# Performance work log

Hardware: AMD Instinct MI355X
Metric: run time of the kernel (lower is better)

The kernel has to match this reference:

```python
import math
import jax, jax.numpy as jnp
import numpy as np

B, T, E, NH = 2, 4096, 768, 12
HS = E // NH

def setup_inputs() -> dict:
    key = jax.random.key(0)
    k1, k2, k3 = jax.random.split(key, 3)
    x = jax.random.normal(k1, (B, T, E), dtype=jnp.float32)
    W_attn = jax.random.normal(k2, (E, 3 * E), dtype=jnp.float32) * (1.0 / math.sqrt(E))
    b_attn = jnp.zeros((3 * E,), dtype=jnp.float32)
    W_proj = jax.random.normal(k3, (E, E), dtype=jnp.float32) * (1.0 / math.sqrt(E))
    b_proj = jnp.zeros((E,), dtype=jnp.float32)
    return {"x": x, "W_attn": W_attn, "b_attn": b_attn, "W_proj": W_proj, "b_proj": b_proj}

def reference(x, W_attn, b_attn, W_proj, b_proj):
    b, t, e = x.shape
    nh, hs = NH, e // NH
    # QKV projection; split order matches einops '(a nh hs)' with a=3 outermost
    qkv = x @ W_attn + b_attn                      # [b, t, 3e]
    qkv = qkv.reshape(b, t, 3, nh, hs)
    q, k, v = jnp.moveaxis(qkv, 2, 0)              # each [b, t, nh, hs]
    q = jnp.transpose(q, (0, 2, 1, 3))             # [b, nh, t, hs]
    k = jnp.transpose(k, (0, 2, 1, 3))
    v = jnp.transpose(v, (0, 2, 1, 3))
    attn = jnp.einsum('bnth,bnsh->bnts', q, k) * (1.0 / math.sqrt(hs))  # [b, nh, t, t]
    causal = jnp.tril(jnp.ones((t, t), dtype=bool))
    attn = jnp.where(causal[None, None], attn, jnp.float32(-jnp.inf))
    attn = jax.nn.softmax(attn, axis=-1)
    y = jnp.einsum('bnts,bnsh->bnth', attn, v)     # [b, nh, t, hs]
    y = jnp.transpose(y, (0, 2, 1, 3)).reshape(b, t, e)
    return y @ W_proj + b_proj
```

## Files before the change

kernel.cpp:

```cpp
#include <hip/hip_runtime.h>
#include <hip/hip_bf16.h>
#include <cmath>

#define B_   2
#define T_   4096
#define E_   768
#define NH_  12
#define HS_  64
#define QKV_ROW (3 * E_)
#define LSE_N (B_ * NH_ * T_)
#define BTE   (B_ * T_ * E_)

typedef __attribute__((ext_vector_type(8))) short bf16x8;
typedef __attribute__((ext_vector_type(4))) float f32x4;

__device__ __forceinline__ unsigned short f2bf(float f) {
    __hip_bfloat16 h = __float2bfloat16(f);
    return __builtin_bit_cast(unsigned short, h);
}
__device__ __forceinline__ float bf2f(unsigned short s) {
    unsigned int u = (unsigned int)s << 16;
    return __builtin_bit_cast(float, u);
}

#define GLOAD16(gptr, lptr)                                             \
    __builtin_amdgcn_global_load_lds(                                   \
        (const __attribute__((address_space(1))) void*)(gptr),          \
        (__attribute__((address_space(3))) void*)(lptr), 16, 0, 0)

__global__ __launch_bounds__(256) void cvt_x_kernel(
    const float* __restrict__ x, unsigned short* __restrict__ xb)
{
    const int i = (blockIdx.x * 256 + threadIdx.x) * 8;
    const float4 v0 = *(const float4*)&x[i];
    const float4 v1 = *(const float4*)&x[i + 4];
    unsigned short o[8];
    o[0] = f2bf(v0.x); o[1] = f2bf(v0.y); o[2] = f2bf(v0.z); o[3] = f2bf(v0.w);
    o[4] = f2bf(v1.x); o[5] = f2bf(v1.y); o[6] = f2bf(v1.z); o[7] = f2bf(v1.w);
    *(int4*)&xb[i] = *(const int4*)o;
}

__global__ __launch_bounds__(256) void transpose_w_kernel(
    const float* __restrict__ W, unsigned short* __restrict__ Wt, int K, int N)
{
    __shared__ float tile[64][65];
    const int k0  = blockIdx.y * 64;
    const int n0  = blockIdx.x * 64;
    const int tid = threadIdx.x;
    const int tc  = tid & 15;
    const int tr  = tid >> 4;
#pragma unroll
    for (int i = 0; i < 4; ++i) {
        const int k = tr + i * 16;
        const float4 v = *(const float4*)&W[(size_t)(k0 + k) * N + n0 + tc * 4];
        tile[k][tc * 4 + 0] = v.x; tile[k][tc * 4 + 1] = v.y;
        tile[k][tc * 4 + 2] = v.z; tile[k][tc * 4 + 3] = v.w;
    }
    __syncthreads();
    const int nr = tid >> 2;
    const int kc = (tid & 3) * 16;
    unsigned short o[16];
#pragma unroll
    for (int j = 0; j < 16; ++j) o[j] = f2bf(tile[kc + j][nr]);
    unsigned short* dst = &Wt[(size_t)(n0 + nr) * K + k0 + kc];
    *(int4*)dst       = *(const int4*)&o[0];
    *(int4*)(dst + 8) = *(const int4*)&o[8];
}

template<bool OUT_BF16, bool QSCALE>
__global__ __launch_bounds__(256) void gemm_bt_kernel(
    const unsigned short* __restrict__ A,
    const unsigned short* __restrict__ Bt,
    const float* __restrict__ bias, void* __restrict__ Cout,
    int M, int N, int K, int lda)
{
    __shared__ __align__(16) unsigned short Als[128 * 64];
    __shared__ __align__(16) unsigned short Bls[128 * 64];

    const int tid  = threadIdx.x;
    const int m0   = blockIdx.y * 128;
    const int n0   = blockIdx.x * 128;
    const int w    = tid >> 6;
    const int lane = tid & 63;
    const int lr   = lane & 15;
    const int lk   = lane >> 4;
    const int wm   = (w >> 1) * 64;
    const int wn   = (w & 1) * 64;

    f32x4 acc[4][4];
#pragma unroll
    for (int i = 0; i < 4; ++i)
#pragma unroll
        for (int j = 0; j < 4; ++j) acc[i][j] = (f32x4){0.f, 0.f, 0.f, 0.f};

    for (int k0 = 0; k0 < K; k0 += 64) {
        __syncthreads();
#pragma unroll
        for (int c = 0; c < 4; ++c) {
            const int idx = c * 256 + tid;
            const int row = idx >> 3;
            const int g   = (tid & 7) ^ (row & 7);
            GLOAD16(&A[(size_t)(m0 + row) * lda + k0 + g * 8], &Als[idx * 8]);
        }
#pragma unroll
        for (int c = 0; c < 4; ++c) {
            const int idx = c * 256 + tid;
            const int row = idx >> 3;
            const int g   = (tid & 7) ^ (row & 7);
            GLOAD16(&Bt[(size_t)(n0 + row) * K + k0 + g * 8], &Bls[idx * 8]);
        }
        __syncthreads();

#pragma unroll
        for (int kk = 0; kk < 2; ++kk) {
            bf16x8 a[4], b[4];
            const int gp = ((kk * 4 + lk) ^ (lr & 7)) << 3;
#pragma unroll
            for (int i = 0; i < 4; ++i) {
                a[i] = *(const bf16x8*)&Als[(wm + i * 16 + lr) * 64 + gp];
                b[i] = *(const bf16x8*)&Bls[(wn + i * 16 + lr) * 64 + gp];
            }
#pragma unroll
            for (int i = 0; i < 4; ++i)
#pragma unroll
                for (int j = 0; j < 4; ++j)
                    acc[i][j] = __builtin_amdgcn_mfma_f32_16x16x32_bf16(
                        a[i], b[j], acc[i][j], 0, 0, 0);
        }
    }

    const float beta = 0.18033688011f;
#pragma unroll
    for (int i = 0; i < 4; ++i) {
#pragma unroll
        for (int j = 0; j < 4; ++j) {
            const int col = n0 + wn + j * 16 + lr;
#pragma unroll
            for (int r = 0; r < 4; ++r) {
                const int row = m0 + wm + i * 16 + lk * 4 + r;
                float v = acc[i][j][r] + bias[col];
                if (QSCALE && col < E_) v *= beta;
                if (OUT_BF16)
                    ((unsigned short*)Cout)[(size_t)row * N + col] = f2bf(v);
                else
                    ((float*)Cout)[(size_t)row * N + col] = v;
            }
        }
    }
}

__global__ __launch_bounds__(256) void flash_kernel(
    const unsigned short* __restrict__ qkv,
    unsigned short* __restrict__ y_part,
    float* __restrict__ lse)
{
    __shared__ __align__(16) unsigned short Kls[64 * 64];
    __shared__ __align__(16) unsigned short Vt[64][72];

    const int tid  = threadIdx.x;
    const int w    = tid >> 6;
    const int lane = tid & 63;
    const int lr   = lane & 15;
    const int lk   = lane >> 4;
    const int head = blockIdx.y;
    const int z    = blockIdx.z;
    const int b    = head / NH_;
    const int nh   = head % NH_;
    const int qb_lo = blockIdx.x;
    const int qb_hi = 63 - qb_lo;
    const int q0_lo = qb_lo * 64;
    const int q0_hi = qb_hi * 64;

    const unsigned short* qkv_b = qkv + (size_t)b * T_ * QKV_ROW;

    bf16x8 qf_lo[2], qf_hi[2];
    {
        const unsigned short* qrl =
            qkv_b + (size_t)(q0_lo + w * 16 + lr) * QKV_ROW + nh * HS_;
        qf_lo[0] = *(const bf16x8*)(qrl + lk * 8);
        qf_lo[1] = *(const bf16x8*)(qrl + 32 + lk * 8);
        const unsigned short* qrh =
            qkv_b + (size_t)(q0_hi + w * 16 + lr) * QKV_ROW + nh * HS_;
        qf_hi[0] = *(const bf16x8*)(qrh + lk * 8);
        qf_hi[1] = *(const bf16x8*)(qrh + 32 + lk * 8);
    }

    bf16x8 af1;
    {
        const short one = (lr == 0) ? (short)0x3F80 : (short)0;
#pragma unroll
        for (int j = 0; j < 8; ++j) af1[j] = one;
    }

    f32x4 acc_lo[4], acc_hi[4];
    f32x4 accl_lo = (f32x4){0.f, 0.f, 0.f, 0.f};
    f32x4 accl_hi = (f32x4){0.f, 0.f, 0.f, 0.f};
#pragma unroll
    for (int i = 0; i < 4; ++i) {
        acc_lo[i] = (f32x4){0.f, 0.f, 0.f, 0.f};
        acc_hi[i] = (f32x4){0.f, 0.f, 0.f, 0.f};
    }
    float m_lo = -INFINITY, m_hi = -INFINITY;

    const int sr = tid >> 2;
    const int sc = (tid & 3) * 16;

    auto softmax_pack = [&](f32x4* st, f32x4* acc, f32x4& accl, float& m,
                            int q0, int kv0, bool diag,
                            bf16x8& pf0, bf16x8& pf1) {
        const int tq = q0 + w * 16 + lr;
        if (diag) {
#pragma unroll
            for (int cb = 0; cb < 4; ++cb)
#pragma unroll
                for (int r = 0; r < 4; ++r) {
                    const int tk = kv0 + cb * 16 + lk * 4 + r;
                    if (tk > tq) st[cb][r] = -INFINITY;
                }
        }
        float mx = -INFINITY;
#pragma unroll
        for (int cb = 0; cb < 4; ++cb)
#pragma unroll
            for (int r = 0; r < 4; ++r) mx = fmaxf(mx, st[cb][r]);
        mx = fmaxf(mx, __shfl_xor(mx, 16));
        mx = fmaxf(mx, __shfl_xor(mx, 32));
        if (__any(mx > m + 8.0f)) {
            const float mnew  = fmaxf(m, mx);
            const float alpha = exp2f(m - mnew);
#pragma unroll
            for (int cb2 = 0; cb2 < 4; ++cb2) acc[cb2] *= alpha;
            accl *= alpha;
            m = mnew;
        }
#pragma unroll
        for (int r = 0; r < 4; ++r) {
            pf0[r]     = (short)f2bf(exp2f(st[0][r] - m));
            pf0[r + 4] = (short)f2bf(exp2f(st[1][r] - m));
            pf1[r]     = (short)f2bf(exp2f(st[2][r] - m));
            pf1[r + 4] = (short)f2bf(exp2f(st[3][r] - m));
        }
    };

    int4 v01r, v23r;
    auto load_vregs = [&](int j) {
        const unsigned short* vrow =
            qkv_b + (size_t)(j * 64 + sr) * QKV_ROW + 2 * E_ + nh * HS_ + sc;
        v01r = *(const int4*)vrow;
        v23r = *(const int4*)(vrow + 8);
    };

    load_vregs(z);
    for (int j = z; j <= qb_hi; ) {
        const int kv0 = j * 64;
        const bool do_lo = (j <= qb_lo);
        __syncthreads();
        {
#pragma unroll
            for (int c = 0; c < 2; ++c) {
                const int idx = c * 256 + tid;
                const int row = idx >> 3;
                const int g   = (tid & 7) ^ (row & 7);
                GLOAD16(&qkv_b[(size_t)(kv0 + row) * QKV_ROW + E_ + nh * HS_ + g * 8],
                        &Kls[idx * 8]);
            }
            const unsigned short* vs0 = (const unsigned short*)&v01r;
            const unsigned short* vs1 = (const unsigned short*)&v23r;
            const int kvhi = sr >> 3, kvlo = sr & 7;
#pragma unroll
            for (int i = 0; i < 8; ++i) {
                const int h = sc + i;
                Vt[h][((kvhi ^ (h >> 3)) << 3) + kvlo] = vs0[i];
            }
#pragma unroll
            for (int i = 0; i < 8; ++i) {
                const int h = sc + 8 + i;
                Vt[h][((kvhi ^ (h >> 3)) << 3) + kvlo] = vs1[i];
            }
        }
        __syncthreads();

        const int jn = j + 2;
        if (jn <= qb_hi) load_vregs(jn);

        bf16x8 pf0h, pf1h, pf0l, pf1l;

        f32x4 st[4];
        __builtin_amdgcn_s_setprio(1);
#pragma unroll
        for (int cb = 0; cb < 4; ++cb) {
            const int rbase = (cb * 16 + lr) * 64;
            const bf16x8 kf0 = *(const bf16x8*)&Kls[rbase + ((lk ^ (lr & 7)) << 3)];
            const bf16x8 kf1 = *(const bf16x8*)&Kls[rbase + (((4 + lk) ^ (lr & 7)) << 3)];
            f32x4 t = (f32x4){0.f, 0.f, 0.f, 0.f};
            t = __builtin_amdgcn_mfma_f32_16x16x32_bf16(kf0, qf_hi[0], t, 0, 0, 0);
            st[cb] = __builtin_amdgcn_mfma_f32_16x16x32_bf16(kf1, qf_hi[1], t, 0, 0, 0);
        }
        __builtin_amdgcn_s_setprio(0);
        softmax_pack(st, acc_hi, accl_hi, m_hi, q0_hi, kv0, j == qb_hi, pf0h, pf1h);
        __builtin_amdgcn_sched_barrier(0);

        if (do_lo) {
            __builtin_amdgcn_s_setprio(1);
#pragma unroll
            for (int cb = 0; cb < 4; ++cb) {
                const int rbase = (cb * 16 + lr) * 64;
                const bf16x8 kf0 = *(const bf16x8*)&Kls[rbase + ((lk ^ (lr & 7)) << 3)];
                const bf16x8 kf1 = *(const bf16x8*)&Kls[rbase + (((4 + lk) ^ (lr & 7)) << 3)];
                f32x4 t = (f32x4){0.f, 0.f, 0.f, 0.f};
                t = __builtin_amdgcn_mfma_f32_16x16x32_bf16(kf0, qf_lo[0], t, 0, 0, 0);
                st[cb] = __builtin_amdgcn_mfma_f32_16x16x32_bf16(kf1, qf_lo[1], t, 0, 0, 0);
            }
            __builtin_amdgcn_s_setprio(0);
            softmax_pack(st, acc_lo, accl_lo, m_lo, q0_lo, kv0, j == qb_lo, pf0l, pf1l);
        }
        __builtin_amdgcn_sched_barrier(0);

        __builtin_amdgcn_s_setprio(1);
#pragma unroll
        for (int cb2 = 0; cb2 < 4; ++cb2) {
            const int row = cb2 * 16 + lr;
            const int sw  = row >> 3;
            bf16x8 vf0, vf1;
#pragma unroll
            for (int ks = 0; ks < 2; ++ks) {
                const int cA = ((4 * ks + (lk >> 1)) ^ sw);
                const int cB = ((4 * ks + 2 + (lk >> 1)) ^ sw);
                const int off = 4 * (lk & 1);
                ushort4 a = *(const ushort4*)&Vt[row][cA * 8 + off];
                ushort4 bq = *(const ushort4*)&Vt[row][cB * 8 + off];
                bf16x8 v;
                v[0] = (short)a.x;  v[1] = (short)a.y;
                v[2] = (short)a.z;  v[3] = (short)a.w;
                v[4] = (short)bq.x; v[5] = (short)bq.y;
                v[6] = (short)bq.z; v[7] = (short)bq.w;
                if (ks == 0) vf0 = v; else vf1 = v;
            }
            acc_hi[cb2] = __builtin_amdgcn_mfma_f32_16x16x32_bf16(vf0, pf0h, acc_hi[cb2], 0, 0, 0);
            acc_hi[cb2] = __builtin_amdgcn_mfma_f32_16x16x32_bf16(vf1, pf1h, acc_hi[cb2], 0, 0, 0);
            if (do_lo) {
                acc_lo[cb2] = __builtin_amdgcn_mfma_f32_16x16x32_bf16(vf0, pf0l, acc_lo[cb2], 0, 0, 0);
                acc_lo[cb2] = __builtin_amdgcn_mfma_f32_16x16x32_bf16(vf1, pf1l, acc_lo[cb2], 0, 0, 0);
            }
        }
        accl_hi = __builtin_amdgcn_mfma_f32_16x16x32_bf16(af1, pf0h, accl_hi, 0, 0, 0);
        accl_hi = __builtin_amdgcn_mfma_f32_16x16x32_bf16(af1, pf1h, accl_hi, 0, 0, 0);
        if (do_lo) {
            accl_lo = __builtin_amdgcn_mfma_f32_16x16x32_bf16(af1, pf0l, accl_lo, 0, 0, 0);
            accl_lo = __builtin_amdgcn_mfma_f32_16x16x32_bf16(af1, pf1l, accl_lo, 0, 0, 0);
        }
        __builtin_amdgcn_s_setprio(0);
        j = jn;
    }

    {
        const float lh = __shfl(accl_hi[0], lr);
        const float ll = __shfl(accl_lo[0], lr);
        unsigned short* yp = y_part + (size_t)z * BTE;
        const float li_hi = (lh > 0.f) ? 1.0f / lh : 0.f;
        const float li_lo = (ll > 0.f) ? 1.0f / ll : 0.f;
        const int tq_hi = q0_hi + w * 16 + lr;
        const int tq_lo = q0_lo + w * 16 + lr;
        unsigned short* yh = &yp[(size_t)(b * T_ + tq_hi) * E_ + nh * HS_];
        unsigned short* yl = &yp[(size_t)(b * T_ + tq_lo) * E_ + nh * HS_];
#pragma unroll
        for (int cb2 = 0; cb2 < 4; ++cb2) {
            ushort4 oh, ol;
            oh.x = f2bf(acc_hi[cb2][0] * li_hi); oh.y = f2bf(acc_hi[cb2][1] * li_hi);
            oh.z = f2bf(acc_hi[cb2][2] * li_hi); oh.w = f2bf(acc_hi[cb2][3] * li_hi);
            ol.x = f2bf(acc_lo[cb2][0] * li_lo); ol.y = f2bf(acc_lo[cb2][1] * li_lo);
            ol.z = f2bf(acc_lo[cb2][2] * li_lo); ol.w = f2bf(acc_lo[cb2][3] * li_lo);
            *(ushort4*)&yh[cb2 * 16 + lk * 4] = oh;
            *(ushort4*)&yl[cb2 * 16 + lk * 4] = ol;
        }
        if (lk == 0) {
            float* lz = lse + (size_t)z * LSE_N + (size_t)head * T_;
            lz[tq_hi] = (lh > 0.f) ? (m_hi + log2f(lh)) : -1e30f;
            lz[tq_lo] = (ll > 0.f) ? (m_lo + log2f(ll)) : -1e30f;
        }
    }
}

__global__ __launch_bounds__(256) void merge_kernel(
    const unsigned short* __restrict__ y_part,
    const float* __restrict__ lse,
    unsigned short* __restrict__ qkv)
{
    const int i  = blockIdx.x * 256 + threadIdx.x;
    const int e0 = i * 8;
    const int row = e0 / E_;
    const int e   = e0 - row * E_;
    const int nh  = e >> 6;
    const int lidx = ((row >> 12) * NH_ + nh) * T_ + (row & (T_ - 1));
    const float s0 = lse[lidx];
    const float s1 = lse[LSE_N + lidx];
    const float M  = fmaxf(s0, s1);
    float w0 = exp2f(s0 - M), w1 = exp2f(s1 - M);
    const float inv = 1.0f / (w0 + w1);
    w0 *= inv; w1 *= inv;
    bf16x8 p0 = *(const bf16x8*)&y_part[e0];
    bf16x8 p1 = *(const bf16x8*)&y_part[(size_t)BTE + e0];
    ushort4 oa, ob;
    unsigned short o[8];
#pragma unroll
    for (int jj = 0; jj < 8; ++jj)
        o[jj] = f2bf(w0 * bf2f((unsigned short)p0[jj]) +
                     w1 * bf2f((unsigned short)p1[jj]));
    oa.x = o[0]; oa.y = o[1]; oa.z = o[2]; oa.w = o[3];
    ob.x = o[4]; ob.y = o[5]; ob.z = o[6]; ob.w = o[7];
    unsigned short* dst = &qkv[(size_t)row * QKV_ROW + e];
    *(ushort4*)dst = oa;
    *(ushort4*)(dst + 4) = ob;
}

extern "C" void kernel_launch(void* const* d_in, const int* in_sizes, int n_in,
                              void* d_out, int out_size, void* d_ws, size_t ws_size,
                              hipStream_t stream)
{
    const float* x      = (const float*)d_in[0];
    const float* W_attn = (const float*)d_in[1];
    const float* b_attn = (const float*)d_in[2];
    const float* W_proj = (const float*)d_in[3];
    const float* b_proj = (const float*)d_in[4];
    float* out = (float*)d_out;

    char* ws = (char*)d_ws;
    unsigned short* qkv_ws  = (unsigned short*)ws;
    float*          lse_ws  = (float*)(ws + 37748736);
    unsigned short* x_bf16  = (unsigned short*)(ws + 38535168);
    unsigned short* wt_attn = (unsigned short*)(ws + 51118080);
    unsigned short* wt_proj = (unsigned short*)(ws + 54657024);
    unsigned short* y_part  = (unsigned short*)d_out;

    dim3 blk(256);

    cvt_x_kernel<<<dim3(BTE / 8 / 256), blk, 0, stream>>>(x, x_bf16);
    transpose_w_kernel<<<dim3(QKV_ROW / 64, E_ / 64), blk, 0, stream>>>(W_attn, wt_attn, E_, QKV_ROW);
    transpose_w_kernel<<<dim3(E_ / 64, E_ / 64), blk, 0, stream>>>(W_proj, wt_proj, E_, E_);

    gemm_bt_kernel<true, true><<<dim3(QKV_ROW / 128, (B_ * T_) / 128), blk, 0, stream>>>(
        x_bf16, wt_attn, b_attn, (void*)qkv_ws, B_ * T_, QKV_ROW, E_, E_);

    flash_kernel<<<dim3(T_ / 128, B_ * NH_, 2), blk, 0, stream>>>(qkv_ws, y_part, lse_ws);

    merge_kernel<<<dim3(BTE / 8 / 256), blk, 0, stream>>>(y_part, lse_ws, qkv_ws);

    gemm_bt_kernel<false, false><<<dim3(E_ / 128, (B_ * T_) / 128), blk, 0, stream>>>(
        qkv_ws, wt_proj, b_proj, (void*)out, B_ * T_, E_, E_, QKV_ROW);
}
```

Baseline: 247.2 us.

## Double-buffer K tiles in LDS and fuse hi/lo QK^T with shared K fragments

Doubles the K shared-memory buffer so the async global-to-LDS load of the next K tile is issued right after the barrier and overlaps the current tile's compute, instead of loading at the start of each iteration. The hi and lo query-block QK^T MFMAs now share a single read of the K fragments from LDS. The sched_barriers between the two softmax phases are removed, giving the compiler more freedom to interleave work. Costs are 8KB more LDS per block, which could lower occupancy, and more live registers from keeping two score arrays at once.

After: 267.2 us. 1.08x slower.

```diff
diff --git a/kernel.cpp b/kernel.cpp
--- a/kernel.cpp
+++ b/kernel.cpp
@@ -154,7 +154,7 @@
     unsigned short* __restrict__ y_part,
     float* __restrict__ lse)
 {
-    __shared__ __align__(16) unsigned short Kls[64 * 64];
+    __shared__ __align__(16) unsigned short Kls[2 * 64 * 64];
     __shared__ __align__(16) unsigned short Vt[64][72];
 
     const int tid  = threadIdx.x;
@@ -242,6 +242,16 @@
         }
     };
 
+    auto issue_k = [&](int j, int buf) {
+#pragma unroll
+        for (int c = 0; c < 2; ++c) {
+            const int idx = c * 256 + tid;
+            const int row = idx >> 3;
+            const int g   = (tid & 7) ^ (row & 7);
+            GLOAD16(&qkv_b[(size_t)(j * 64 + row) * QKV_ROW + E_ + nh * HS_ + g * 8],
+                    &Kls[buf * 4096 + idx * 8]);
+        }
+    };
     int4 v01r, v23r;
     auto load_vregs = [&](int j) {
         const unsigned short* vrow =
@@ -250,20 +260,14 @@
         v23r = *(const int4*)(vrow + 8);
     };
 
+    issue_k(z, 0);
     load_vregs(z);
-    for (int j = z; j <= qb_hi; ) {
+    int cur = 0;
+    for (int j = z; j <= qb_hi; j += 2, cur ^= 1) {
         const int kv0 = j * 64;
         const bool do_lo = (j <= qb_lo);
         __syncthreads();
         {
-#pragma unroll
-            for (int c = 0; c < 2; ++c) {
-                const int idx = c * 256 + tid;
-                const int row = idx >> 3;
-                const int g   = (tid & 7) ^ (row & 7);
-                GLOAD16(&qkv_b[(size_t)(kv0 + row) * QKV_ROW + E_ + nh * HS_ + g * 8],
-                        &Kls[idx * 8]);
-            }
             const unsigned short* vs0 = (const unsigned short*)&v01r;
             const unsigned short* vs1 = (const unsigned short*)&v23r;
             const int kvhi = sr >> 3, kvlo = sr & 7;
@@ -281,40 +285,35 @@
         __syncthreads();
 
         const int jn = j + 2;
-        if (jn <= qb_hi) load_vregs(jn);
-
-        bf16x8 pf0h, pf1h, pf0l, pf1l;
-
-        f32x4 st[4];
+        if (jn <= qb_hi) {
+            issue_k(jn, cur ^ 1);
+            load_vregs(jn);
+        }
+
+        const unsigned short* Kb = &Kls[cur * 4096];
+
+        f32x4 st_hi[4], st_lo[4];
         __builtin_amdgcn_s_setprio(1);
 #pragma unroll
         for (int cb = 0; cb < 4; ++cb) {
             const int rbase = (cb * 16 + lr) * 64;
-            const bf16x8 kf0 = *(const bf16x8*)&Kls[rbase + ((lk ^ (lr & 7)) << 3)];
-            const bf16x8 kf1 = *(const bf16x8*)&Kls[rbase + (((4 + lk) ^ (lr & 7)) << 3)];
+            const bf16x8 kf0 = *(const bf16x8*)&Kb[rbase + ((lk ^ (lr & 7)) << 3)];
+            const bf16x8 kf1 = *(const bf16x8*)&Kb[rbase + (((4 + lk) ^ (lr & 7)) << 3)];
             f32x4 t = (f32x4){0.f, 0.f, 0.f, 0.f};
             t = __builtin_amdgcn_mfma_f32_16x16x32_bf16(kf0, qf_hi[0], t, 0, 0, 0);
-            st[cb] = __builtin_amdgcn_mfma_f32_16x16x32_bf16(kf1, qf_hi[1], t, 0, 0, 0);
+            st_hi[cb] = __builtin_amdgcn_mfma_f32_16x16x32_bf16(kf1, qf_hi[1], t, 0, 0, 0);
+            if (do_lo) {
+                f32x4 u = (f32x4){0.f, 0.f, 0.f, 0.f};
+                u = __builtin_amdgcn_mfma_f32_16x16x32_bf16(kf0, qf_lo[0], u, 0, 0, 0);
+                st_lo[cb] = __builtin_amdgcn_mfma_f32_16x16x32_bf16(kf1, qf_lo[1], u, 0, 0, 0);
+            }
         }
         __builtin_amdgcn_s_setprio(0);
-        softmax_pack(st, acc_hi, accl_hi, m_hi, q0_hi, kv0, j == qb_hi, pf0h, pf1h);
-        __builtin_amdgcn_sched_barrier(0);
-
-        if (do_lo) {
-            __builtin_amdgcn_s_setprio(1);
-#pragma unroll
-            for (int cb = 0; cb < 4; ++cb) {
-                const int rbase = (cb * 16 + lr) * 64;
-                const bf16x8 kf0 = *(const bf16x8*)&Kls[rbase + ((lk ^ (lr & 7)) << 3)];
-                const bf16x8 kf1 = *(const bf16x8*)&Kls[rbase + (((4 + lk) ^ (lr & 7)) << 3)];
-                f32x4 t = (f32x4){0.f, 0.f, 0.f, 0.f};
-                t = __builtin_amdgcn_mfma_f32_16x16x32_bf16(kf0, qf_lo[0], t, 0, 0, 0);
-                st[cb] = __builtin_amdgcn_mfma_f32_16x16x32_bf16(kf1, qf_lo[1], t, 0, 0, 0);
-            }
-            __builtin_amdgcn_s_setprio(0);
-            softmax_pack(st, acc_lo, accl_lo, m_lo, q0_lo, kv0, j == qb_lo, pf0l, pf1l);
-        }
-        __builtin_amdgcn_sched_barrier(0);
+
+        bf16x8 pf0h, pf1h, pf0l, pf1l;
+        softmax_pack(st_hi, acc_hi, accl_hi, m_hi, q0_hi, kv0, j == qb_hi, pf0h, pf1h);
+        if (do_lo)
+            softmax_pack(st_lo, acc_lo, accl_lo, m_lo, q0_lo, kv0, j == qb_lo, pf0l, pf1l);
 
         __builtin_amdgcn_s_setprio(1);
 #pragma unroll
@@ -350,7 +349,6 @@
             accl_lo = __builtin_amdgcn_mfma_f32_16x16x32_bf16(af1, pf1l, accl_lo, 0, 0, 0);
         }
         __builtin_amdgcn_s_setprio(0);
-        j = jn;
     }
 
     {
```
